# Performance work log

Measured on AMD Instinct MI355X. Metric: run time of the kernel, lower is better.

## Reference

```python
import jax, jax.numpy as jnp
import numpy as np

SIGMA = 32.0
EPS = 1e-8

def setup_inputs() -> dict:
    key = jax.random.key(0)
    k1, k2, k3 = jax.random.split(key, 3)
    N, D, O = 8192, 512, 512
    x = jax.random.normal(k1, (N, D), dtype=jnp.float32)
    # Linear params (kaiming-normal-ish init represented as scaled normals)
    W = jax.random.normal(k2, (O, D), dtype=jnp.float32) * (2.0 / D) ** 0.5
    b = jnp.zeros((O,), dtype=jnp.float32)
    return {"x": x, "W": W, "b": b}

def reference(x, W, b):
    # squared pairwise L2 distances via the Gram trick: ||xi||^2 + ||xj||^2 - 2 xi.xj
    sq = jnp.sum(x * x, axis=-1)                      # [N]
    sqd = sq[:, None] + sq[None, :] - 2.0 * (x @ x.T)  # [N, N]
    sqd = jnp.maximum(sqd, 0.0)                        # numerical clamp (cdist >= 0)
    weights = jnp.exp(-sqd / (2.0 * SIGMA * SIGMA))    # Gaussian kernel [N, N]
    weights = weights / (jnp.sum(weights, axis=1, keepdims=True) + EPS)
    output = weights @ x                               # Nadaraya-Watson weighted avg [N, D]
    return output @ W.T + b                            # linear head [N, O]
```

## Files before the change

### kernel.cpp

```cpp
#include <hip/hip_runtime.h>
#include <stdint.h>

#define NPTS 8192
#define DIM  512
#define ODIM 512

typedef __attribute__((ext_vector_type(8))) short short8;
typedef __attribute__((ext_vector_type(4))) float f32x4;

__device__ __forceinline__ void gload_lds16(const void* g, void* l) {
  __builtin_amdgcn_global_load_lds(
      (__attribute__((address_space(1))) void*)g,
      (__attribute__((address_space(3))) void*)l, 16, 0, 0);
}

__device__ __forceinline__ short f2bf(float f) {
  uint32_t u = __float_as_uint(f);
  u = (u + 0x7FFFu + ((u >> 16) & 1u)) >> 16;
  return (short)u;
}

__device__ __forceinline__ void gemm_core_nt(const short* __restrict__ A,
                                             const short* __restrict__ B,
                                             int K, int lda, int ldb,
                                             short* smem, f32x4 acc[4][4]) {
  const int tid  = threadIdx.x;
  const int wid  = tid >> 6;
  const int lane = tid & 63;
  const int wr = wid >> 1, wc = wid & 1;
  const int sr = lane >> 2;
  const int sc = (lane & 3) << 3;
  const int fr = lane & 15, fg = lane >> 4;
  short* sA = smem;
  short* sB = smem + 4096;
  short* dA0 = sA + wid * 512;
  short* dA1 = sA + 2048 + wid * 512;
  short* dB0 = sB + wid * 512;
  short* dB1 = sB + 2048 + wid * 512;
  const short* pa0 = A + (size_t)(wid * 16 + sr) * lda + sc;
  const short* pa1 = A + (size_t)(64 + wid * 16 + sr) * lda + sc;
  const short* pb0 = B + (size_t)(wid * 16 + sr) * ldb + sc;
  const short* pb1 = B + (size_t)(64 + wid * 16 + sr) * ldb + sc;

  for (int k0 = 0; k0 < K; k0 += 32) {
    gload_lds16(pa0 + k0, dA0);
    gload_lds16(pa1 + k0, dA1);
    gload_lds16(pb0 + k0, dB0);
    gload_lds16(pb1 + k0, dB1);
    __syncthreads();
    short8 af[4], bb[4];
#pragma unroll
    for (int m = 0; m < 4; ++m)
      af[m] = *(const short8*)(sA + (wr * 64 + m * 16 + fr) * 32 + fg * 8);
#pragma unroll
    for (int n = 0; n < 4; ++n)
      bb[n] = *(const short8*)(sB + (wc * 64 + n * 16 + fr) * 32 + fg * 8);
#pragma unroll
    for (int m = 0; m < 4; ++m)
#pragma unroll
      for (int n = 0; n < 4; ++n)
        acc[m][n] = __builtin_amdgcn_mfma_f32_16x16x32_bf16(af[m], bb[n], acc[m][n], 0, 0, 0);
    __syncthreads();
  }
}

#define ZERO_ACC(acc)                        \
  {                                          \
    f32x4 _z = {0.f, 0.f, 0.f, 0.f};         \
    _Pragma("unroll")                        \
    for (int m = 0; m < 4; ++m)              \
      _Pragma("unroll")                      \
      for (int n = 0; n < 4; ++n) acc[m][n] = _z; \
  }

__global__ __launch_bounds__(256) void k_prep_x(const float* __restrict__ x,
                                                short* __restrict__ xb,
                                                float* __restrict__ sq) {
  const int row  = blockIdx.x * 4 + (threadIdx.x >> 6);
  const int lane = threadIdx.x & 63;
  const float* px = x + (size_t)row * DIM + lane * 8;
  const float4 v0 = *(const float4*)px;
  const float4 v1 = *(const float4*)(px + 4);
  float s = v0.x*v0.x + v0.y*v0.y + v0.z*v0.z + v0.w*v0.w +
            v1.x*v1.x + v1.y*v1.y + v1.z*v1.z + v1.w*v1.w;
  short8 o;
  o[0]=f2bf(v0.x); o[1]=f2bf(v0.y); o[2]=f2bf(v0.z); o[3]=f2bf(v0.w);
  o[4]=f2bf(v1.x); o[5]=f2bf(v1.y); o[6]=f2bf(v1.z); o[7]=f2bf(v1.w);
  *(short8*)(xb + (size_t)row * DIM + lane * 8) = o;
#pragma unroll
  for (int m = 32; m >= 1; m >>= 1) s += __shfl_xor(s, m);
  if (lane == 0) sq[row] = s;
}

__global__ __launch_bounds__(256) void k_prep_w(const float* __restrict__ W,
                                                short* __restrict__ Wb) {
  const int idx = blockIdx.x * 256 + threadIdx.x;
  const float4 v0 = *(const float4*)(W + (size_t)idx * 8);
  const float4 v1 = *(const float4*)(W + (size_t)idx * 8 + 4);
  short8 o;
  o[0]=f2bf(v0.x); o[1]=f2bf(v0.y); o[2]=f2bf(v0.z); o[3]=f2bf(v0.w);
  o[4]=f2bf(v1.x); o[5]=f2bf(v1.y); o[6]=f2bf(v1.z); o[7]=f2bf(v1.w);
  *(short8*)(Wb + (size_t)idx * 8) = o;
}

__global__ __launch_bounds__(256) void k_ybt(const short* __restrict__ xb,
                                             const short* __restrict__ Wb,
                                             short* __restrict__ YbT) {
  __shared__ short smem[8192];
  f32x4 acc[4][4];
  ZERO_ACC(acc);
  const int rowBase = blockIdx.y * 128;
  const int colBase = blockIdx.x * 128;
  gemm_core_nt(Wb + (size_t)rowBase * DIM, xb + (size_t)colBase * DIM,
               DIM, DIM, DIM, smem, acc);
  const int lane = threadIdx.x & 63, wid = threadIdx.x >> 6;
  const int wr = wid >> 1, wc = wid & 1, fr = lane & 15, fg = lane >> 4;
#pragma unroll
  for (int m = 0; m < 4; ++m)
#pragma unroll
    for (int n = 0; n < 4; ++n)
#pragma unroll
      for (int r = 0; r < 4; ++r) {
        const int ro = rowBase + wr * 64 + m * 16 + fg * 4 + r;
        const int ci = colBase + wc * 64 + n * 16 + fr;
        YbT[(size_t)ro * NPTS + ci] = f2bf(acc[m][n][r]);
      }
}

__global__ __launch_bounds__(256) void k_pmat(const short* __restrict__ xb,
                                              const float* __restrict__ sq,
                                              short* __restrict__ P,
                                              float* __restrict__ rowsum,
                                              int jbase, int SW) {
  __shared__ short smem[8192];
  f32x4 acc[4][4];
  ZERO_ACC(acc);
  const int rowBase = blockIdx.y * 128;
  const int colTile = blockIdx.x * 128;
  const int jglob = jbase + colTile;
  gemm_core_nt(xb + (size_t)rowBase * DIM, xb + (size_t)jglob * DIM,
               DIM, DIM, DIM, smem, acc);
  const int lane = threadIdx.x & 63, wid = threadIdx.x >> 6;
  const int wr = wid >> 1, wc = wid & 1, fr = lane & 15, fg = lane >> 4;
  float sj[4];
#pragma unroll
  for (int n = 0; n < 4; ++n) sj[n] = sq[jglob + wc * 64 + n * 16 + fr];
#pragma unroll
  for (int m = 0; m < 4; ++m) {
#pragma unroll
    for (int r = 0; r < 4; ++r) {
      const int i = rowBase + wr * 64 + m * 16 + fg * 4 + r;
      const float si = sq[i];
      float rs = 0.f;
#pragma unroll
      for (int n = 0; n < 4; ++n) {
        const float t = fminf(2.f * acc[m][n][r] - si - sj[n], 0.f) * (1.0f / 2048.0f);
        const float w = __expf(t);
        rs += w;
        P[(size_t)i * SW + (colTile + wc * 64 + n * 16 + fr)] = f2bf(w);
      }
      rs += __shfl_xor(rs, 1);
      rs += __shfl_xor(rs, 2);
      rs += __shfl_xor(rs, 4);
      rs += __shfl_xor(rs, 8);
      if (fr == 0) atomicAdd(&rowsum[i], rs);
    }
  }
}

__global__ __launch_bounds__(256) void k_pv(const short* __restrict__ P,
                                            const short* __restrict__ YbT,
                                            float* __restrict__ out_acc,
                                            int jbase, int SW, int klen) {
  __shared__ short smem[8192];
  f32x4 acc[4][4];
  ZERO_ACC(acc);
  const int rowBase = blockIdx.y * 128;
  const int colBase = blockIdx.x * 128;
  const int kz = blockIdx.z * klen;
  gemm_core_nt(P + (size_t)rowBase * SW + kz,
               YbT + (size_t)colBase * NPTS + jbase + kz,
               klen, SW, NPTS, smem, acc);
  const int lane = threadIdx.x & 63, wid = threadIdx.x >> 6;
  const int wr = wid >> 1, wc = wid & 1, fr = lane & 15, fg = lane >> 4;
#pragma unroll
  for (int m = 0; m < 4; ++m)
#pragma unroll
    for (int n = 0; n < 4; ++n)
#pragma unroll
      for (int r = 0; r < 4; ++r) {
        const int i = rowBase + wr * 64 + m * 16 + fg * 4 + r;
        const int o = colBase + wc * 64 + n * 16 + fr;
        atomicAdd(&out_acc[(size_t)i * ODIM + o], acc[m][n][r]);
      }
}

__global__ __launch_bounds__(256) void k_final(const float* __restrict__ out_acc,
                                               const float* __restrict__ rowsum,
                                               const float* __restrict__ bvec,
                                               float* __restrict__ out) {
  const int idx = blockIdx.x * 256 + threadIdx.x;
  const int i = idx >> 7;
  const int o = (idx & 127) << 2;
  const float inv = 1.f / (rowsum[i] + 1e-8f);
  const float4 a = *(const float4*)(out_acc + (size_t)i * ODIM + o);
  const float4 bb = *(const float4*)(bvec + o);
  float4 r;
  r.x = a.x * inv + bb.x;
  r.y = a.y * inv + bb.y;
  r.z = a.z * inv + bb.z;
  r.w = a.w * inv + bb.w;
  *(float4*)(out + (size_t)i * ODIM + o) = r;
}

extern "C" void kernel_launch(void* const* d_in, const int* in_sizes, int n_in,
                              void* d_out, int out_size, void* d_ws, size_t ws_size,
                              hipStream_t stream) {
  (void)in_sizes; (void)n_in; (void)out_size;
  const float* x = (const float*)d_in[0];
  const float* W = (const float*)d_in[1];
  const float* bvec = (const float*)d_in[2];
  float* out = (float*)d_out;
  char* ws = (char*)d_ws;

  short* xb      = (short*)(ws + 0);
  short* Wb      = (short*)(ws + 8388608);
  short* YbT     = (short*)(ws + 8912896);
  float* sq      = (float*)(ws + 17301504);
  float* rowsum  = (float*)(ws + 17334272);
  float* out_acc = (float*)(ws + 17367040);
  short* P       = (short*)(ws + 34144256);

  size_t pav = ws_size > 34144256 ? ws_size - 34144256 : 0;
  int SW = 8192;
  while (SW > 128 && (size_t)NPTS * SW * 2 > pav) SW >>= 1;
  const int nstrips = NPTS / SW;
  int ksplit = SW / 2048;
  if (ksplit < 1) ksplit = 1;
  if (ksplit > 4) ksplit = 4;
  const int klen = SW / ksplit;

  hipMemsetAsync(rowsum, 0, NPTS * sizeof(float), stream);
  hipMemsetAsync(out_acc, 0, (size_t)NPTS * ODIM * sizeof(float), stream);

  k_prep_x<<<dim3(NPTS / 4), 256, 0, stream>>>(x, xb, sq);
  k_prep_w<<<dim3(ODIM * DIM / 8 / 256), 256, 0, stream>>>(W, Wb);
  k_ybt<<<dim3(NPTS / 128, ODIM / 128), 256, 0, stream>>>(xb, Wb, YbT);

  for (int s = 0; s < nstrips; ++s) {
    const int jbase = s * SW;
    k_pmat<<<dim3(SW / 128, NPTS / 128), 256, 0, stream>>>(xb, sq, P, rowsum, jbase, SW);
    k_pv<<<dim3(ODIM / 128, NPTS / 128, ksplit), 256, 0, stream>>>(P, YbT, out_acc, jbase, SW, klen);
  }

  k_final<<<dim3(NPTS * ODIM / 4 / 256), 256, 0, stream>>>(out_acc, rowsum, bvec, out);
}
```

Measured before the change: 407.8 us.

## Use 256x256 double-buffered GEMM tiles with 8 waves for pmat and pv

Adds a new GEMM core that gives each 512-thread block a 256x256 output tile with BK=64. Global-to-LDS loads go into two 64KB-total buffers, so the next K slice is staged while the current one is computed. The Gram/exp kernel and the P@Y kernel both switch to it, which raises arithmetic intensity per LDS/global load and removes one barrier per iteration. In exchange each block uses more registers and the full 128KB LDS, and the grids get smaller, which risks lower occupancy and poorer wave balance on the GPU.

```diff
diff --git a/kernel.cpp b/kernel.cpp
--- a/kernel.cpp
+++ b/kernel.cpp
@@ -19,6 +19,78 @@
   u = (u + 0x7FFFu + ((u >> 16) & 1u)) >> 16;
   return (short)u;
 }
+
+__device__ __forceinline__ void gemm256_2ph(const short* __restrict__ A,
+                                            const short* __restrict__ B,
+                                            int K, int lda, int ldb,
+                                            short* lds, f32x4 acc[8][4]) {
+  const int tid  = threadIdx.x;
+  const int wid  = tid >> 6;
+  const int lane = tid & 63;
+  const int wr = wid >> 2, wc = wid & 3;
+  const int fr = lane & 15, fg = lane >> 4;
+  const int srow = lane >> 3;
+  const int scol = (lane & 7) << 3;
+
+  const short* sa[4];
+  const short* sb[4];
+  int da[4];
+#pragma unroll
+  for (int q = 0; q < 4; ++q) {
+    const int gi = q * 8 + wid;
+    sa[q] = A + (size_t)(gi * 8 + srow) * lda + scol;
+    sb[q] = B + (size_t)(gi * 8 + srow) * ldb + scol;
+    da[q] = gi * 512;
+  }
+
+  auto stage = [&](int bo, int k0) {
+#pragma unroll
+    for (int q = 0; q < 4; ++q) gload_lds16(sa[q] + k0, lds + bo + da[q]);
+#pragma unroll
+    for (int q = 0; q < 4; ++q) gload_lds16(sb[q] + k0, lds + bo + 16384 + da[q]);
+  };
+
+  auto compute = [&](int bo) {
+    const short* sA = lds + bo;
+    const short* sB = lds + bo + 16384;
+#pragma unroll
+    for (int kk = 0; kk < 2; ++kk) {
+      short8 af[8], bb[4];
+#pragma unroll
+      for (int m = 0; m < 8; ++m)
+        af[m] = *(const short8*)(sA + (wr * 128 + m * 16 + fr) * 64 + kk * 32 + fg * 8);
+#pragma unroll
+      for (int n = 0; n < 4; ++n)
+        bb[n] = *(const short8*)(sB + (wc * 64 + n * 16 + fr) * 64 + kk * 32 + fg * 8);
+#pragma unroll
+      for (int m = 0; m < 8; ++m)
+#pragma unroll
+        for (int n = 0; n < 4; ++n)
+          acc[m][n] = __builtin_amdgcn_mfma_f32_16x16x32_bf16(af[m], bb[n], acc[m][n], 0, 0, 0);
+    }
+  };
+
+  stage(0, 0);
+  __syncthreads();
+  int bo = 0;
+  const int nt = K >> 6;
+  for (int t = 0; t < nt - 1; ++t) {
+    stage(bo ^ 32768, (t + 1) << 6);
+    compute(bo);
+    __syncthreads();
+    bo ^= 32768;
+  }
+  compute(bo);
+}
+
+#define ZERO_ACC8(acc)                       \
+  {                                          \
+    f32x4 _z = {0.f, 0.f, 0.f, 0.f};         \
+    _Pragma("unroll")                        \
+    for (int m = 0; m < 8; ++m)              \
+      _Pragma("unroll")                      \
+      for (int n = 0; n < 4; ++n) acc[m][n] = _z; \
+  }
 
 __device__ __forceinline__ void gemm_core_nt(const short* __restrict__ A,
                                              const short* __restrict__ B,
@@ -64,7 +136,7 @@
   }
 }
 
-#define ZERO_ACC(acc)                        \
+#define ZERO_ACC4(acc)                       \
   {                                          \
     f32x4 _z = {0.f, 0.f, 0.f, 0.f};         \
     _Pragma("unroll")                        \
@@ -108,7 +180,7 @@
                                              short* __restrict__ YbT) {
   __shared__ short smem[8192];
   f32x4 acc[4][4];
-  ZERO_ACC(acc);
+  ZERO_ACC4(acc);
   const int rowBase = blockIdx.y * 128;
   const int colBase = blockIdx.x * 128;
   gemm_core_nt(Wb + (size_t)rowBase * DIM, xb + (size_t)colBase * DIM,
@@ -127,29 +199,29 @@
       }
 }
 
-__global__ __launch_bounds__(256) void k_pmat(const short* __restrict__ xb,
-                                              const float* __restrict__ sq,
-                                              short* __restrict__ P,
-                                              float* __restrict__ rowsum,
-                                              int jbase, int SW) {
-  __shared__ short smem[8192];
-  f32x4 acc[4][4];
-  ZERO_ACC(acc);
-  const int rowBase = blockIdx.y * 128;
-  const int colTile = blockIdx.x * 128;
+__global__ __launch_bounds__(512, 2) void k_pmat(const short* __restrict__ xb,
+                                                 const float* __restrict__ sq,
+                                                 short* __restrict__ P,
+                                                 float* __restrict__ rowsum,
+                                                 int jbase, int SW) {
+  __shared__ short lds[65536];
+  f32x4 acc[8][4];
+  ZERO_ACC8(acc);
+  const int rowBase = blockIdx.y * 256;
+  const int colTile = blockIdx.x * 256;
   const int jglob = jbase + colTile;
-  gemm_core_nt(xb + (size_t)rowBase * DIM, xb + (size_t)jglob * DIM,
-               DIM, DIM, DIM, smem, acc);
+  gemm256_2ph(xb + (size_t)rowBase * DIM, xb + (size_t)jglob * DIM,
+              DIM, DIM, DIM, lds, acc);
   const int lane = threadIdx.x & 63, wid = threadIdx.x >> 6;
-  const int wr = wid >> 1, wc = wid & 1, fr = lane & 15, fg = lane >> 4;
+  const int wr = wid >> 2, wc = wid & 3, fr = lane & 15, fg = lane >> 4;
   float sj[4];
 #pragma unroll
   for (int n = 0; n < 4; ++n) sj[n] = sq[jglob + wc * 64 + n * 16 + fr];
 #pragma unroll
-  for (int m = 0; m < 4; ++m) {
+  for (int m = 0; m < 8; ++m) {
 #pragma unroll
     for (int r = 0; r < 4; ++r) {
-      const int i = rowBase + wr * 64 + m * 16 + fg * 4 + r;
+      const int i = rowBase + wr * 128 + m * 16 + fg * 4 + r;
       const float si = sq[i];
       float rs = 0.f;
 #pragma unroll
@@ -168,28 +240,28 @@
   }
 }
 
-__global__ __launch_bounds__(256) void k_pv(const short* __restrict__ P,
-                                            const short* __restrict__ YbT,
-                                            float* __restrict__ out_acc,
-                                            int jbase, int SW, int klen) {
-  __shared__ short smem[8192];
-  f32x4 acc[4][4];
-  ZERO_ACC(acc);
-  const int rowBase = blockIdx.y * 128;
-  const int colBase = blockIdx.x * 128;
+__global__ __launch_bounds__(512, 2) void k_pv(const short* __restrict__ P,
+                                               const short* __restrict__ YbT,
+                                               float* __restrict__ out_acc,
+                                               int jbase, int SW, int klen) {
+  __shared__ short lds[65536];
+  f32x4 acc[8][4];
+  ZERO_ACC8(acc);
+  const int rowBase = blockIdx.y * 256;
+  const int colBase = blockIdx.x * 256;
   const int kz = blockIdx.z * klen;
-  gemm_core_nt(P + (size_t)rowBase * SW + kz,
-               YbT + (size_t)colBase * NPTS + jbase + kz,
-               klen, SW, NPTS, smem, acc);
+  gemm256_2ph(P + (size_t)rowBase * SW + kz,
+              YbT + (size_t)colBase * NPTS + jbase + kz,
+              klen, SW, NPTS, lds, acc);
   const int lane = threadIdx.x & 63, wid = threadIdx.x >> 6;
-  const int wr = wid >> 1, wc = wid & 1, fr = lane & 15, fg = lane >> 4;
-#pragma unroll
-  for (int m = 0; m < 4; ++m)
+  const int wr = wid >> 2, wc = wid & 3, fr = lane & 15, fg = lane >> 4;
+#pragma unroll
+  for (int m = 0; m < 8; ++m)
 #pragma unroll
     for (int n = 0; n < 4; ++n)
 #pragma unroll
       for (int r = 0; r < 4; ++r) {
-        const int i = rowBase + wr * 64 + m * 16 + fg * 4 + r;
+        const int i = rowBase + wr * 128 + m * 16 + fg * 4 + r;
         const int o = colBase + wc * 64 + n * 16 + fr;
         atomicAdd(&out_acc[(size_t)i * ODIM + o], acc[m][n][r]);
       }
@@ -233,7 +305,7 @@
 
   size_t pav = ws_size > 34144256 ? ws_size - 34144256 : 0;
   int SW = 8192;
-  while (SW > 128 && (size_t)NPTS * SW * 2 > pav) SW >>= 1;
+  while (SW > 256 && (size_t)NPTS * SW * 2 > pav) SW >>= 1;
   const int nstrips = NPTS / SW;
   int ksplit = SW / 2048;
   if (ksplit < 1) ksplit = 1;
@@ -249,8 +321,8 @@
 
   for (int s = 0; s < nstrips; ++s) {
     const int jbase = s * SW;
-    k_pmat<<<dim3(SW / 128, NPTS / 128), 256, 0, stream>>>(xb, sq, P, rowsum, jbase, SW);
-    k_pv<<<dim3(ODIM / 128, NPTS / 128, ksplit), 256, 0, stream>>>(P, YbT, out_acc, jbase, SW, klen);
+    k_pmat<<<dim3(SW / 256, NPTS / 256), 512, 0, stream>>>(xb, sq, P, rowsum, jbase, SW);
+    k_pv<<<dim3(ODIM / 256, NPTS / 256, ksplit), 512, 0, stream>>>(P, YbT, out_acc, jbase, SW, klen);
   }
 
   k_final<<<dim3(NPTS * ODIM / 4 / 256), 256, 0, stream>>>(out_acc, rowsum, bvec, out);
```

Measured after the change: 360.5 us. 1.13x faster.

## Exploit distance-matrix symmetry and use K=64 swizzled LDS GEMM tiles

Applied to the files above, without the earlier changes.

The P-matrix kernel now launches only the upper-triangular 128x128 tiles when the full strip fits. Each off-diagonal tile writes both itself and its transpose, staged through a swizzled LDS buffer, and adds column sums into rowsum. The intent is to roughly halve the Gram GEMM and exp work. A new GEMM core with K-step 64 and XOR-swizzled LDS layout replaces the K=32 core for the P and PV kernels, which cuts sync count and bank conflicts. The cost is more LDS per block, a serial tile-index decode loop, and strided LDS reads for the transpose writeback.

```diff
diff --git a/kernel.cpp b/kernel.cpp
--- a/kernel.cpp
+++ b/kernel.cpp
@@ -19,6 +19,67 @@
   u = (u + 0x7FFFu + ((u >> 16) & 1u)) >> 16;
   return (short)u;
 }
+
+__device__ __forceinline__ void gemm128(const short* __restrict__ A,
+                                        const short* __restrict__ B,
+                                        int K, int lda, int ldb,
+                                        short* lds, f32x4 acc[4][4]) {
+  const int tid = threadIdx.x, wid = tid >> 6, lane = tid & 63;
+  const int wr = wid >> 1, wc = wid & 1, fr = lane & 15, fg = (lane >> 4) & 3;
+  const int nt = K >> 6;
+  const short* srcA[4]; const short* srcB[4]; int dst[4];
+#pragma unroll
+  for (int u = 0; u < 4; ++u) {
+    const int g = u * 256 + tid;
+    const int r = g >> 3;
+    const int cl = (g & 7) ^ (r & 7);
+    srcA[u] = A + (size_t)r * lda + cl * 8;
+    srcB[u] = B + (size_t)r * ldb + cl * 8;
+    dst[u] = (u * 256 + wid * 64) * 8;
+  }
+  short* sB = lds + 8192;
+  const int c0 = (fg ^ (fr & 7)) * 8;
+  const int c1 = ((4 + fg) ^ (fr & 7)) * 8;
+
+  for (int t = 0; t < nt; ++t) {
+    const int k0 = t << 6;
+#pragma unroll
+    for (int u = 0; u < 4; ++u) gload_lds16(srcA[u] + k0, lds + dst[u]);
+#pragma unroll
+    for (int u = 0; u < 4; ++u) gload_lds16(srcB[u] + k0, sB + dst[u]);
+    __syncthreads();
+    short8 af[4][2], bb[4][2];
+#pragma unroll
+    for (int m = 0; m < 4; ++m) {
+      const int rr = (wr * 64 + m * 16 + fr) * 64;
+      af[m][0] = *(const short8*)(lds + rr + c0);
+      af[m][1] = *(const short8*)(lds + rr + c1);
+    }
+#pragma unroll
+    for (int n = 0; n < 4; ++n) {
+      const int rr = (wc * 64 + n * 16 + fr) * 64;
+      bb[n][0] = *(const short8*)(sB + rr + c0);
+      bb[n][1] = *(const short8*)(sB + rr + c1);
+    }
+#pragma unroll
+    for (int kk = 0; kk < 2; ++kk)
+#pragma unroll
+      for (int m = 0; m < 4; ++m)
+#pragma unroll
+        for (int n = 0; n < 4; ++n)
+          acc[m][n] = __builtin_amdgcn_mfma_f32_16x16x32_bf16(af[m][kk], bb[n][kk], acc[m][n], 0, 0, 0);
+    __syncthreads();
+  }
+}
+
+#define ZERO_ACC4(acc)                       \
+  {                                          \
+    f32x4 _z = {0.f, 0.f, 0.f, 0.f};         \
+    _Pragma("unroll")                        \
+    for (int m = 0; m < 4; ++m)              \
+      _Pragma("unroll")                      \
+      for (int n = 0; n < 4; ++n) acc[m][n] = _z; \
+  }
 
 __device__ __forceinline__ void gemm_core_nt(const short* __restrict__ A,
                                              const short* __restrict__ B,
@@ -64,15 +125,6 @@
   }
 }
 
-#define ZERO_ACC(acc)                        \
-  {                                          \
-    f32x4 _z = {0.f, 0.f, 0.f, 0.f};         \
-    _Pragma("unroll")                        \
-    for (int m = 0; m < 4; ++m)              \
-      _Pragma("unroll")                      \
-      for (int n = 0; n < 4; ++n) acc[m][n] = _z; \
-  }
-
 __global__ __launch_bounds__(256) void k_prep_x(const float* __restrict__ x,
                                                 short* __restrict__ xb,
                                                 float* __restrict__ sq) {
@@ -108,7 +160,7 @@
                                              short* __restrict__ YbT) {
   __shared__ short smem[8192];
   f32x4 acc[4][4];
-  ZERO_ACC(acc);
+  ZERO_ACC4(acc);
   const int rowBase = blockIdx.y * 128;
   const int colBase = blockIdx.x * 128;
   gemm_core_nt(Wb + (size_t)rowBase * DIM, xb + (size_t)colBase * DIM,
@@ -132,32 +184,44 @@
                                               short* __restrict__ P,
                                               float* __restrict__ rowsum,
                                               int jbase, int SW) {
-  __shared__ short smem[8192];
+  __shared__ short lds[17408];
   f32x4 acc[4][4];
-  ZERO_ACC(acc);
-  const int rowBase = blockIdx.y * 128;
-  const int colTile = blockIdx.x * 128;
-  const int jglob = jbase + colTile;
-  gemm_core_nt(xb + (size_t)rowBase * DIM, xb + (size_t)jglob * DIM,
-               DIM, DIM, DIM, smem, acc);
-  const int lane = threadIdx.x & 63, wid = threadIdx.x >> 6;
-  const int wr = wid >> 1, wc = wid & 1, fr = lane & 15, fg = lane >> 4;
-  float sj[4];
-#pragma unroll
-  for (int n = 0; n < 4; ++n) sj[n] = sq[jglob + wc * 64 + n * 16 + fr];
+  ZERO_ACC4(acc);
+  int bi, bj; bool mirror;
+  if (gridDim.y > 1) {
+    bi = blockIdx.y; bj = blockIdx.x; mirror = false;
+  } else {
+    int n = blockIdx.x; bi = 0;
+    while (n >= 64 - bi) { n -= 64 - bi; ++bi; }
+    bj = bi + n; mirror = (bj != bi);
+  }
+  const int rowBase = bi * 128;
+  const int colOff  = bj * 128;
+  const int jglob   = jbase + colOff;
+  gemm128(xb + (size_t)rowBase * DIM, xb + (size_t)jglob * DIM,
+          DIM, DIM, DIM, lds, acc);
+
+  const int tid = threadIdx.x, lane = tid & 63, wid = tid >> 6;
+  const int wr = wid >> 1, wc = wid & 1, fr = lane & 15, fg = (lane >> 4) & 3;
+  float sjv[4];
+#pragma unroll
+  for (int n = 0; n < 4; ++n) sjv[n] = sq[jglob + wc * 64 + n * 16 + fr];
+  float cs[4] = {0.f, 0.f, 0.f, 0.f};
 #pragma unroll
   for (int m = 0; m < 4; ++m) {
 #pragma unroll
     for (int r = 0; r < 4; ++r) {
-      const int i = rowBase + wr * 64 + m * 16 + fg * 4 + r;
+      const int il = wr * 64 + m * 16 + fg * 4 + r;
+      const int i  = rowBase + il;
       const float si = sq[i];
       float rs = 0.f;
 #pragma unroll
       for (int n = 0; n < 4; ++n) {
-        const float t = fminf(2.f * acc[m][n][r] - si - sj[n], 0.f) * (1.0f / 2048.0f);
+        const float t = fminf(2.f * acc[m][n][r] - si - sjv[n], 0.f) * (1.0f / 2048.0f);
         const float w = __expf(t);
-        rs += w;
-        P[(size_t)i * SW + (colTile + wc * 64 + n * 16 + fr)] = f2bf(w);
+        rs += w; cs[n] += w;
+        const int jl = wc * 64 + n * 16 + fr;
+        lds[il * 136 + (((jl >> 3) ^ (il & 7)) << 3) + (jl & 7)] = f2bf(w);
       }
       rs += __shfl_xor(rs, 1);
       rs += __shfl_xor(rs, 2);
@@ -166,23 +230,55 @@
       if (fr == 0) atomicAdd(&rowsum[i], rs);
     }
   }
+  if (mirror) {
+#pragma unroll
+    for (int n = 0; n < 4; ++n) {
+      cs[n] += __shfl_xor(cs[n], 16);
+      cs[n] += __shfl_xor(cs[n], 32);
+    }
+    if (lane < 16) {
+#pragma unroll
+      for (int n = 0; n < 4; ++n)
+        atomicAdd(&rowsum[jglob + wc * 64 + n * 16 + lane], cs[n]);
+    }
+  }
+  __syncthreads();
+#pragma unroll
+  for (int v = 0; v < 8; ++v) {
+    const int g = v * 256 + tid;
+    const int rl = g >> 4, c = g & 15;
+    short8 val = *(const short8*)(lds + rl * 136 + ((c ^ (rl & 7)) << 3));
+    *(short8*)(P + (size_t)(rowBase + rl) * SW + colOff + c * 8) = val;
+  }
+  if (mirror) {
+#pragma unroll
+    for (int v = 0; v < 8; ++v) {
+      const int g = v * 256 + tid;
+      const int jl = g >> 4, ci = g & 15;
+      short8 o;
+#pragma unroll
+      for (int e = 0; e < 8; ++e)
+        o[e] = lds[(ci * 8 + e) * 136 + ((((jl >> 3) ^ e)) << 3) + (jl & 7)];
+      *(short8*)(P + (size_t)(jglob + jl) * SW + rowBase + ci * 8) = o;
+    }
+  }
 }
 
 __global__ __launch_bounds__(256) void k_pv(const short* __restrict__ P,
                                             const short* __restrict__ YbT,
                                             float* __restrict__ out_acc,
                                             int jbase, int SW, int klen) {
-  __shared__ short smem[8192];
+  __shared__ short lds[16384];
   f32x4 acc[4][4];
-  ZERO_ACC(acc);
+  ZERO_ACC4(acc);
   const int rowBase = blockIdx.y * 128;
   const int colBase = blockIdx.x * 128;
   const int kz = blockIdx.z * klen;
-  gemm_core_nt(P + (size_t)rowBase * SW + kz,
-               YbT + (size_t)colBase * NPTS + jbase + kz,
-               klen, SW, NPTS, smem, acc);
+  gemm128(P + (size_t)rowBase * SW + kz,
+          YbT + (size_t)colBase * NPTS + jbase + kz,
+          klen, SW, NPTS, lds, acc);
   const int lane = threadIdx.x & 63, wid = threadIdx.x >> 6;
-  const int wr = wid >> 1, wc = wid & 1, fr = lane & 15, fg = lane >> 4;
+  const int wr = wid >> 1, wc = wid & 1, fr = lane & 15, fg = (lane >> 4) & 3;
 #pragma unroll
   for (int m = 0; m < 4; ++m)
 #pragma unroll
@@ -249,7 +345,11 @@
 
   for (int s = 0; s < nstrips; ++s) {
     const int jbase = s * SW;
-    k_pmat<<<dim3(SW / 128, NPTS / 128), 256, 0, stream>>>(xb, sq, P, rowsum, jbase, SW);
+    if (SW == 8192) {
+      k_pmat<<<dim3(2080, 1), 256, 0, stream>>>(xb, sq, P, rowsum, 0, SW);
+    } else {
+      k_pmat<<<dim3(SW / 128, NPTS / 128), 256, 0, stream>>>(xb, sq, P, rowsum, jbase, SW);
+    }
     k_pv<<<dim3(ODIM / 128, NPTS / 128, ksplit), 256, 0, stream>>>(P, YbT, out_acc, jbase, SW, klen);
   }
 
```

After: 358.4 us. 12.1% less time.
